# Kernel tuning notes

Hardware: AMD Instinct MI355X
Metric: run time of the kernel (lower is better)

## Reference

```python
import jax, jax.numpy as jnp
import numpy as np

N_NODES = 100000
N_EDGES = 1600000
FEAT_DIM = 64
IN_DIM = FEAT_DIM + 3  # feat + xyz


def setup_inputs() -> dict:
    key = jax.random.key(0)
    k1, k2, k3, k4, k5 = jax.random.split(key, 5)
    xyz = jax.random.normal(k1, (N_NODES, 3), dtype=jnp.float32)
    feat = jax.random.normal(k2, (N_NODES, FEAT_DIM), dtype=jnp.float32)
    edge_index = jax.random.randint(k3, (2, N_EDGES), 0, N_NODES, dtype=jnp.int64)
    # MLP params (Linear stored as [in, out] for x @ W + b)
    W1 = jax.random.normal(k4, (2 * IN_DIM, FEAT_DIM), dtype=jnp.float32) * (1.0 / np.sqrt(2 * IN_DIM))
    b1 = jnp.zeros((FEAT_DIM,), dtype=jnp.float32)
    W2 = jax.random.normal(k5, (FEAT_DIM, FEAT_DIM), dtype=jnp.float32) * (1.0 / np.sqrt(FEAT_DIM))
    b2 = jnp.zeros((FEAT_DIM,), dtype=jnp.float32)
    return {"xyz": xyz, "feat": feat, "edge_index": edge_index,
            "W1": W1, "b1": b1, "W2": W2, "b2": b2}


def reference(xyz, feat, edge_index, W1, b1, W2, b2):
    # node features: cat([feat, xyz]) -> [N, C+3]
    x = jnp.concatenate([feat, xyz], axis=-1)
    src = edge_index[0]  # j (source / neighbor)
    dst = edge_index[1]  # i (target, aggregation index)
    x_i = x[dst]                       # [E, C+3]
    x_j = x[src]                       # [E, C+3]
    # EdgeConv message: mlp(cat([x_i, x_j - x_i]))
    m = jnp.concatenate([x_i, x_j - x_i], axis=-1)   # [E, 2*(C+3)]
    h = jax.nn.relu(m @ W1 + b1) @ W2 + b2           # [E, C]
    n = x.shape[0]
    agg = jax.ops.segment_max(h, dst, num_segments=n)  # [N, C]
    # nodes with no incoming edges get 0 (matches PyG scatter-max fill)
    deg = jax.ops.segment_sum(jnp.ones((dst.shape[0],), h.dtype), dst, num_segments=n)
    return jnp.where(deg[:, None] > 0, agg, jnp.zeros_like(agg))
```

## Files before the change

### kernel.cpp

```cpp
#include <hip/hip_runtime.h>
#include <stdint.h>

#define N_NODES 100000
#define FEAT 64
#define NB 64
#define SC_CHUNK 8192
#define NBKT 1563
#define BKT_CAP 1400
#define RVN 6
#define BIAS 512.0f

typedef __attribute__((ext_vector_type(8))) _Float16 half8;
typedef __attribute__((ext_vector_type(2))) _Float16 half2v;
typedef __attribute__((ext_vector_type(2))) __fp16 fp16x2;
typedef __attribute__((ext_vector_type(4))) float f32x4;

__device__ __forceinline__ uint32_t enc_key(float f) {
    uint32_t u = __float_as_uint(f);
    return (u & 0x80000000u) ? ~u : (u | 0x80000000u);
}
__device__ __forceinline__ float dec_key(uint32_t k) {
    return __uint_as_float((k & 0x80000000u) ? (k & 0x7FFFFFFFu) : ~k);
}
__device__ __forceinline__ uint32_t pk_f16(float a, float b) {
    union { fp16x2 h; uint32_t u; } cv;
    cv.h = __builtin_amdgcn_cvt_pkrtz(a, b);
    return cv.u;
}

#define W2T_OFF 0
#define AMB_OFF 4096
#define BM_OFF  8384
#define W2P_OFF 12672
#define U_OFF   16384
#define V_OFF   (U_OFF + N_NODES * FEAT / 2)
#define GCNT_OFF (U_OFF + N_NODES * FEAT)
#define SRT_OFF  (GCNT_OFF + 2048)

__global__ __launch_bounds__(256) void transform_kernel(
    const float* __restrict__ W1, const float* __restrict__ W2,
    float* __restrict__ ws, int full)
{
    int i = blockIdx.x * 256 + threadIdx.x;
    if (full && i < 2048)
        ((uint32_t*)ws)[GCNT_OFF + i] = 0u;
    if (i < 4096) {
        int c2 = i >> 6, c = i & 63;
        ws[W2T_OFF + i] = W2[c * 64 + c2];
    } else if (full && i < 8384) {
        int j = i - 4096;
        ws[AMB_OFF + j] = W1[j] - W1[j + 67 * 64];
    } else if (full && i < 12672) {
        int j = i - 8384;
        ws[BM_OFF + j] = W1[j + 67 * 64];
    } else if (full && i < 16768) {
        int p = i - 12672;
        int j = p & 7, c2lo = (p >> 3) & 15, quad = (p >> 7) & 3;
        int h = (p >> 9) & 1, n4 = (p >> 10) & 3;
        int k = h * 32 + quad * 8 + j;
        int n = n4 * 16 + c2lo;
        ((_Float16*)(ws + W2P_OFF))[p] = (_Float16)W2[k * 64 + n];
    }
}

__global__ __launch_bounds__(256, 4) void nodebkt_kernel(
    const float* __restrict__ xyz, const float* __restrict__ feat,
    const float* __restrict__ b1, const float* __restrict__ ws,
    uint16_t* __restrict__ U, uint16_t* __restrict__ V, int nN,
    const int* __restrict__ ei, uint32_t* __restrict__ gcnt,
    uint32_t* __restrict__ sorted, int nE, int nBkt)
{
    __shared__ uint32_t hist[NBKT];

    int t = threadIdx.x;

    if ((int)blockIdx.x < nBkt) {
        int e0 = blockIdx.x * SC_CHUNK;
        int cnt = min(SC_CHUNK, nE - e0);
        int cnt4 = cnt & ~3;

        for (int i = t; i < NBKT; i += 256) hist[i] = 0;
        __syncthreads();
        for (int i = t * 4; i < cnt4; i += 1024) {
            uint4 d4 = *(const uint4*)(ei + nE + e0 + i);
            atomicAdd(&hist[d4.x >> 6], 1u);
            atomicAdd(&hist[d4.y >> 6], 1u);
            atomicAdd(&hist[d4.z >> 6], 1u);
            atomicAdd(&hist[d4.w >> 6], 1u);
        }
        for (int i = cnt4 + t; i < cnt; i += 256)
            atomicAdd(&hist[ei[nE + e0 + i] >> 6], 1u);
        __syncthreads();
        for (int b = t; b < NBKT; b += 256) {
            uint32_t c = hist[b];
            hist[b] = c ? atomicAdd(&gcnt[b], c) : 0u;
        }
        __syncthreads();
        for (int i = t * 4; i < cnt4; i += 1024) {
            uint4 s4 = *(const uint4*)(ei + e0 + i);
            uint4 d4 = *(const uint4*)(ei + nE + e0 + i);
            uint32_t sa[4] = {(uint32_t)s4.x, (uint32_t)s4.y, (uint32_t)s4.z, (uint32_t)s4.w};
            uint32_t da[4] = {(uint32_t)d4.x, (uint32_t)d4.y, (uint32_t)d4.z, (uint32_t)d4.w};
            #pragma unroll
            for (int k = 0; k < 4; ++k) {
                uint32_t b = da[k] >> 6;
                uint32_t pos = atomicAdd(&hist[b], 1u);
                if (pos < BKT_CAP)
                    sorted[(size_t)b * BKT_CAP + pos] = sa[k] | ((da[k] & 63u) << 20);
            }
        }
        for (int i = cnt4 + t; i < cnt; i += 256) {
            uint32_t src = (uint32_t)ei[e0 + i];
            uint32_t dst = (uint32_t)ei[nE + e0 + i];
            uint32_t b = dst >> 6;
            uint32_t pos = atomicAdd(&hist[b], 1u);
            if (pos < BKT_CAP)
                sorted[(size_t)b * BKT_CAP + pos] = src | ((dst & 63u) << 20);
        }
        return;
    }

    int nb = blockIdx.x - nBkt;
    int half = nb & 1;
    int n = (nb >> 1) * 256 + t;
    if (n >= nN) return;
    const float* __restrict__ W = ws + (half ? BM_OFF : AMB_OFF);

    float acc[FEAT];
    if (half == 0) {
        #pragma unroll
        for (int c = 0; c < FEAT; ++c) acc[c] = b1[c];
    } else {
        #pragma unroll
        for (int c = 0; c < FEAT; ++c) acc[c] = 0.0f;
    }

    const float* f = feat + (size_t)n * FEAT;
    #pragma unroll 1
    for (int k = 0; k < 64; k += 4) {
        float4 x4 = *(const float4*)(f + k);
        float xv[4] = {x4.x, x4.y, x4.z, x4.w};
        #pragma unroll
        for (int q = 0; q < 4; ++q) {
            const float* __restrict__ w = W + (k + q) * 64;
            #pragma unroll
            for (int c = 0; c < FEAT; ++c)
                acc[c] = fmaf(xv[q], w[c], acc[c]);
        }
    }
    const float* p = xyz + (size_t)n * 3;
    #pragma unroll
    for (int k3 = 0; k3 < 3; ++k3) {
        float xv = p[k3];
        const float* __restrict__ w = W + (64 + k3) * 64;
        #pragma unroll
        for (int c = 0; c < FEAT; ++c)
            acc[c] = fmaf(xv, w[c], acc[c]);
    }
    uint4* outp = (uint4*)((half ? V : U) + (size_t)n * FEAT);
    #pragma unroll
    for (int q = 0; q < 8; ++q) {
        uint4 o;
        o.x = pk_f16(acc[8*q + 0], acc[8*q + 1]);
        o.y = pk_f16(acc[8*q + 2], acc[8*q + 3]);
        o.z = pk_f16(acc[8*q + 4], acc[8*q + 5]);
        o.w = pk_f16(acc[8*q + 6], acc[8*q + 7]);
        outp[q] = o;
    }
}

#define LOADE(G, DSV, VV0, VV1, UU0, UU1) do {                               \
        int e_c_ = min((G) + el, cnt - 1);                                   \
        uint32_t val_ = ssrt[e_c_];                                          \
        DSV = *(const uint4*)(ssrt + (G) + quad * 4);                        \
        int src_ = (int)(val_ & 0xFFFFFu);                                   \
        const uint32_t* vr_ = (const uint32_t*)(V + (size_t)src_ * FEAT);    \
        VV0 = *(const uint4*)(vr_ + quad * 4);                               \
        VV1 = *(const uint4*)(vr_ + 16 + quad * 4);                          \
        const uint32_t* ur_ = ushare + (int)(val_ >> 20) * 32;               \
        UU0 = *(const uint4*)(ur_ + quad * 4);                               \
        UU1 = *(const uint4*)(ur_ + 16 + quad * 4);                          \
    } while (0)

__global__ __launch_bounds__(256) void agg_kernel(
    const uint32_t* __restrict__ gcnt, const uint32_t* __restrict__ sorted,
    const uint16_t* __restrict__ U, const uint16_t* __restrict__ V,
    const float* __restrict__ ws_w2p, const float* __restrict__ b2,
    float* __restrict__ out, int nN)
{
    __shared__ int      lmax[NB * 65];
    __shared__ uint32_t ushare[NB * 32];
    __shared__ uint32_t ssrt[BKT_CAP + 16];
    __shared__ uint32_t shist[NB];

    int bkt = blockIdx.x;
    int nb0 = bkt * NB;
    int rows = min(NB, nN - nb0);
    int cnt = min((int)gcnt[bkt], BKT_CAP);
    int t = threadIdx.x;

    for (int i = t; i < NB * 65; i += 256) lmax[i] = 0;
    if (t < NB) shist[t] = 0;
    {
        const uint4* usrc4 = (const uint4*)(U + (size_t)nb0 * FEAT);
        for (int i = t; i < rows * 8; i += 256) ((uint4*)ushare)[i] = usrc4[i];
    }
    const uint32_t* bsrc = sorted + (size_t)bkt * BKT_CAP;
    __syncthreads();

    uint32_t rv[RVN];
    #pragma unroll
    for (int j = 0; j < RVN; ++j) {
        int i = t + j * 256;
        if (i < cnt) {
            uint32_t v = bsrc[i];
            rv[j] = v;
            atomicAdd(&shist[v >> 20], 1u);
        }
    }
    __syncthreads();
    if (t < NB) {
        uint32_t v = shist[t];
        uint32_t run = v;
        #pragma unroll
        for (int d = 1; d < 64; d <<= 1) {
            uint32_t x = (uint32_t)__shfl_up((int)run, (unsigned)d, 64);
            if (t >= d) run += x;
        }
        shist[t] = run - v;
    }
    __syncthreads();
    #pragma unroll
    for (int j = 0; j < RVN; ++j) {
        int i = t + j * 256;
        if (i < cnt) {
            uint32_t v = rv[j];
            uint32_t pos = atomicAdd(&shist[v >> 20], 1u);
            ssrt[pos] = v;
        }
    }
    __syncthreads();

    int lane = t & 63;
    int wave = t >> 6;
    int el = lane & 15, quad = lane >> 4;

    const uint4* w2p = (const uint4*)ws_w2p;
    union { uint4 u4; half8 h8; } bfr[8];
    #pragma unroll
    for (int q8 = 0; q8 < 8; ++q8)
        bfr[q8].u4 = w2p[(q8 * 4 + quad) * 16 + el];
    float b2v[4];
    #pragma unroll
    for (int n4 = 0; n4 < 4; ++n4) b2v[n4] = b2[n4 * 16 + el] + BIAS;

    const half2v zero2 = {(_Float16)0.0f, (_Float16)0.0f};

    uint4 dsv_c, vv_c0, vv_c1, uu_c0, uu_c1;
    int g = wave * 16;
    if (g < cnt) LOADE(g, dsv_c, vv_c0, vv_c1, uu_c0, uu_c1);

    #pragma unroll 1
    for (; g < cnt; g += 64) {
        int gn = g + 64;
        int gl = (gn < cnt) ? gn : g;
        uint4 dsv_n, vv_n0, vv_n1, uu_n0, uu_n1;
        LOADE(gl, dsv_n, vv_n0, vv_n1, uu_n0, uu_n1);

        union { uint4 u4; half8 h8; } afr[2];
        #pragma unroll
        for (int h = 0; h < 2; ++h) {
            uint4 uu = h ? uu_c1 : uu_c0;
            uint4 vv = h ? vv_c1 : vv_c0;
            uint32_t ua[4] = {uu.x, uu.y, uu.z, uu.w};
            uint32_t va[4] = {vv.x, vv.y, vv.z, vv.w};
            uint32_t pk[4];
            #pragma unroll
            for (int p = 0; p < 4; ++p) {
                union { uint32_t u; half2v h2; } cu, cv2, ct;
                cu.u = ua[p]; cv2.u = va[p];
                ct.h2 = __builtin_elementwise_max(cu.h2 + cv2.h2, zero2);
                pk[p] = ct.u;
            }
            afr[h].u4 = make_uint4(pk[0], pk[1], pk[2], pk[3]);
        }

        f32x4 acc[4];
        #pragma unroll
        for (int n4 = 0; n4 < 4; ++n4)
            acc[n4] = (f32x4){b2v[n4], b2v[n4], b2v[n4], b2v[n4]};
        #pragma unroll
        for (int n4 = 0; n4 < 4; ++n4) {
            acc[n4] = __builtin_amdgcn_mfma_f32_16x16x32_f16(afr[0].h8, bfr[n4*2+0].h8, acc[n4], 0, 0, 0);
            acc[n4] = __builtin_amdgcn_mfma_f32_16x16x32_f16(afr[1].h8, bfr[n4*2+1].h8, acc[n4], 0, 0, 0);
        }

        int d0 = (int)(dsv_c.x >> 20), d1 = (int)(dsv_c.y >> 20);
        int d2 = (int)(dsv_c.z >> 20), d3 = (int)(dsv_c.w >> 20);
        int eb = g + quad * 4;
        bool ok0 = eb < cnt, ok1 = eb + 1 < cnt;
        bool ok2 = eb + 2 < cnt, ok3 = eb + 3 < cnt;
        bool m0 = (d0 == d1) & ok1;
        bool m1 = (d1 == d2) & ok2;
        bool m2 = (d2 == d3) & ok3;
        #pragma unroll
        for (int n4 = 0; n4 < 4; ++n4) {
            if (m0) acc[n4][1] = fmaxf(acc[n4][1], acc[n4][0]);
            if (m1) acc[n4][2] = fmaxf(acc[n4][2], acc[n4][1]);
            if (m2) acc[n4][3] = fmaxf(acc[n4][3], acc[n4][2]);
        }
        if (ok0 & !m0) {
            #pragma unroll
            for (int n4 = 0; n4 < 4; ++n4)
                atomicMax(&lmax[d0 * 65 + n4 * 16 + el], __float_as_int(acc[n4][0]));
        }
        if (ok1 & !m1) {
            #pragma unroll
            for (int n4 = 0; n4 < 4; ++n4)
                atomicMax(&lmax[d1 * 65 + n4 * 16 + el], __float_as_int(acc[n4][1]));
        }
        if (ok2 & !m2) {
            #pragma unroll
            for (int n4 = 0; n4 < 4; ++n4)
                atomicMax(&lmax[d2 * 65 + n4 * 16 + el], __float_as_int(acc[n4][2]));
        }
        if (ok3) {
            #pragma unroll
            for (int n4 = 0; n4 < 4; ++n4)
                atomicMax(&lmax[d3 * 65 + n4 * 16 + el], __float_as_int(acc[n4][3]));
        }

        dsv_c = dsv_n;
        vv_c0 = vv_n0; vv_c1 = vv_n1;
        uu_c0 = uu_n0; uu_c1 = uu_n1;
    }
    __syncthreads();

    for (int i = t * 4; i < rows * FEAT; i += 1024) {
        int r = i >> 6, c = i & 63;
        int lb = r * 65 + c;
        int k0 = lmax[lb + 0], k1 = lmax[lb + 1];
        int k2 = lmax[lb + 2], k3 = lmax[lb + 3];
        float4 o;
        o.x = k0 ? (__int_as_float(k0) - BIAS) : 0.0f;
        o.y = k1 ? (__int_as_float(k1) - BIAS) : 0.0f;
        o.z = k2 ? (__int_as_float(k2) - BIAS) : 0.0f;
        o.w = k3 ? (__int_as_float(k3) - BIAS) : 0.0f;
        *(float4*)(out + (size_t)(nb0 + r) * FEAT + c) = o;
    }
}
#undef LOADE

__device__ __forceinline__ void rank1_update(
    float* __restrict__ h, float xi, float d,
    const float* __restrict__ A, const float* __restrict__ B)
{
    #pragma unroll
    for (int c = 0; c < FEAT; ++c)
        h[c] = fmaf(xi, A[c], fmaf(d, B[c], h[c]));
}

__global__ __launch_bounds__(256) void edge_fused_kernel(
    const float* __restrict__ xyz, const float* __restrict__ feat,
    const int* __restrict__ ei,
    const float* __restrict__ W1, const float* __restrict__ b1,
    const float* __restrict__ ws, const float* __restrict__ b2,
    uint32_t* __restrict__ keys, int nE)
{
    int e = blockIdx.x * 256 + threadIdx.x;
    if (e >= nE) return;
    int src = ei[e];
    int dst = ei[nE + e];
    const float* __restrict__ W2T = ws + W2T_OFF;

    float h[FEAT];
    #pragma unroll
    for (int c = 0; c < FEAT; ++c) h[c] = b1[c];

    const float* fi = feat + (size_t)dst * FEAT;
    const float* fj = feat + (size_t)src * FEAT;
    #pragma unroll 1
    for (int k = 0; k < 64; k += 4) {
        float4 a = *(const float4*)(fi + k);
        float4 b = *(const float4*)(fj + k);
        rank1_update(h, a.x, b.x - a.x, W1 + (k + 0) * 64, W1 + (67 + k + 0) * 64);
        rank1_update(h, a.y, b.y - a.y, W1 + (k + 1) * 64, W1 + (67 + k + 1) * 64);
        rank1_update(h, a.z, b.z - a.z, W1 + (k + 2) * 64, W1 + (67 + k + 2) * 64);
        rank1_update(h, a.w, b.w - a.w, W1 + (k + 3) * 64, W1 + (67 + k + 3) * 64);
    }
    {
        const float* pi = xyz + (size_t)dst * 3;
        const float* pj = xyz + (size_t)src * 3;
        #pragma unroll
        for (int k3 = 0; k3 < 3; ++k3) {
            float xi = pi[k3];
            rank1_update(h, xi, pj[k3] - xi, W1 + (64 + k3) * 64, W1 + (131 + k3) * 64);
        }
    }
    #pragma unroll
    for (int c = 0; c < FEAT; ++c) h[c] = fmaxf(h[c], 0.0f);

    uint32_t* krow = keys + (size_t)dst * FEAT;
    #pragma unroll 1
    for (int c2 = 0; c2 < FEAT; c2 += 4) {
        float o0 = b2[c2 + 0], o1 = b2[c2 + 1];
        float o2 = b2[c2 + 2], o3 = b2[c2 + 3];
        const float* w0 = W2T + (c2 + 0) * 64;
        const float* w1 = W2T + (c2 + 1) * 64;
        const float* w2 = W2T + (c2 + 2) * 64;
        const float* w3 = W2T + (c2 + 3) * 64;
        #pragma unroll
        for (int c = 0; c < FEAT; ++c) {
            float hv = h[c];
            o0 = fmaf(hv, w0[c], o0);
            o1 = fmaf(hv, w1[c], o1);
            o2 = fmaf(hv, w2[c], o2);
            o3 = fmaf(hv, w3[c], o3);
        }
        uint32_t k0 = enc_key(o0), k1 = enc_key(o1);
        uint32_t k2 = enc_key(o2), k3 = enc_key(o3);
        uint4 cur = *(const uint4*)(krow + c2);
        if (k0 > cur.x) atomicMax(&krow[c2 + 0], k0);
        if (k1 > cur.y) atomicMax(&krow[c2 + 1], k1);
        if (k2 > cur.z) atomicMax(&krow[c2 + 2], k2);
        if (k3 > cur.w) atomicMax(&krow[c2 + 3], k3);
    }
}

__global__ __launch_bounds__(256) void decode_kernel(
    uint32_t* __restrict__ keys, int n4)
{
    int i = blockIdx.x * 256 + threadIdx.x;
    if (i >= n4) return;
    uint4 k = ((const uint4*)keys)[i];
    float4 r;
    r.x = k.x ? dec_key(k.x) : 0.0f;
    r.y = k.y ? dec_key(k.y) : 0.0f;
    r.z = k.z ? dec_key(k.z) : 0.0f;
    r.w = k.w ? dec_key(k.w) : 0.0f;
    ((float4*)keys)[i] = r;
}

extern "C" void kernel_launch(void* const* d_in, const int* in_sizes, int n_in,
                              void* d_out, int out_size, void* d_ws, size_t ws_size,
                              hipStream_t stream)
{
    const float* xyz  = (const float*)d_in[0];
    const float* feat = (const float*)d_in[1];
    const int*   ei   = (const int*)d_in[2];
    const float* W1   = (const float*)d_in[3];
    const float* b1   = (const float*)d_in[4];
    const float* W2   = (const float*)d_in[5];
    const float* b2   = (const float*)d_in[6];

    int nE = in_sizes[2] / 2;
    float* ws = (float*)d_ws;

    size_t need_words = (size_t)SRT_OFF + (size_t)NBKT * BKT_CAP;
    int full = (ws_size >= need_words * 4) ? 1 : 0;

    transform_kernel<<<66, 256, 0, stream>>>(W1, W2, ws, full);

    if (full) {
        uint16_t* U = (uint16_t*)(ws + U_OFF);
        uint16_t* V = (uint16_t*)(ws + V_OFF);
        uint32_t* gcnt   = (uint32_t*)(ws + GCNT_OFF);
        uint32_t* sorted = (uint32_t*)(ws + SRT_OFF);

        int nBkt = (nE + SC_CHUNK - 1) / SC_CHUNK;
        int nodeBlocks = ((N_NODES + 255) / 256) * 2;
        nodebkt_kernel<<<nBkt + nodeBlocks, 256, 0, stream>>>(
            xyz, feat, b1, ws, U, V, N_NODES, ei, gcnt, sorted, nE, nBkt);
        agg_kernel<<<NBKT, 256, 0, stream>>>(
            gcnt, sorted, U, V, ws + W2P_OFF, b2, (float*)d_out, N_NODES);
    } else {
        uint32_t* keys = (uint32_t*)d_out;
        hipMemsetAsync(d_out, 0, (size_t)out_size * sizeof(float), stream);
        edge_fused_kernel<<<(nE + 255) / 256, 256, 0, stream>>>(
            xyz, feat, ei, W1, b1, ws, b2, keys, nE);
        decode_kernel<<<(out_size / 4 + 255) / 256, 256, 0, stream>>>(
            keys, out_size / 4);
    }
}
```

Before: 189.5 us.

## Split fused node/bucket kernel into separate launches with LDS occupancy padding

Separates the combined node-projection and edge-bucketing kernel into two kernels launched back to back on the same stream. The node kernel gets a 2D grid and a large dummy shared-memory array, touched only on a never-taken path, that limits blocks per CU, presumably to reduce register or cache pressure from the 64-float accumulator. This removes the branch divergence between block roles and the shared launch bounds, but loses the overlap the fused launch gave between bucketing and node work and adds one launch.

After: 224.6 us. 1.19x slower.

```diff
diff --git a/kernel.cpp b/kernel.cpp
--- a/kernel.cpp
+++ b/kernel.cpp
@@ -9,6 +9,7 @@
 #define BKT_CAP 1400
 #define RVN 6
 #define BIAS 512.0f
+#define NODE_PAD_WORDS 9600
 
 typedef __attribute__((ext_vector_type(8))) _Float16 half8;
 typedef __attribute__((ext_vector_type(2))) _Float16 half2v;
@@ -63,66 +64,22 @@
     }
 }
 
-__global__ __launch_bounds__(256, 4) void nodebkt_kernel(
+__global__ __launch_bounds__(256) void node_kernel(
     const float* __restrict__ xyz, const float* __restrict__ feat,
     const float* __restrict__ b1, const float* __restrict__ ws,
-    uint16_t* __restrict__ U, uint16_t* __restrict__ V, int nN,
-    const int* __restrict__ ei, uint32_t* __restrict__ gcnt,
-    uint32_t* __restrict__ sorted, int nE, int nBkt)
-{
-    __shared__ uint32_t hist[NBKT];
-
+    uint16_t* __restrict__ U, uint16_t* __restrict__ V, int nN)
+{
+    __shared__ uint32_t occ_pad[NODE_PAD_WORDS];
     int t = threadIdx.x;
-
-    if ((int)blockIdx.x < nBkt) {
-        int e0 = blockIdx.x * SC_CHUNK;
-        int cnt = min(SC_CHUNK, nE - e0);
-        int cnt4 = cnt & ~3;
-
-        for (int i = t; i < NBKT; i += 256) hist[i] = 0;
+    if (nN == -1) {
+        occ_pad[t] = (uint32_t)t;
         __syncthreads();
-        for (int i = t * 4; i < cnt4; i += 1024) {
-            uint4 d4 = *(const uint4*)(ei + nE + e0 + i);
-            atomicAdd(&hist[d4.x >> 6], 1u);
-            atomicAdd(&hist[d4.y >> 6], 1u);
-            atomicAdd(&hist[d4.z >> 6], 1u);
-            atomicAdd(&hist[d4.w >> 6], 1u);
-        }
-        for (int i = cnt4 + t; i < cnt; i += 256)
-            atomicAdd(&hist[ei[nE + e0 + i] >> 6], 1u);
-        __syncthreads();
-        for (int b = t; b < NBKT; b += 256) {
-            uint32_t c = hist[b];
-            hist[b] = c ? atomicAdd(&gcnt[b], c) : 0u;
-        }
-        __syncthreads();
-        for (int i = t * 4; i < cnt4; i += 1024) {
-            uint4 s4 = *(const uint4*)(ei + e0 + i);
-            uint4 d4 = *(const uint4*)(ei + nE + e0 + i);
-            uint32_t sa[4] = {(uint32_t)s4.x, (uint32_t)s4.y, (uint32_t)s4.z, (uint32_t)s4.w};
-            uint32_t da[4] = {(uint32_t)d4.x, (uint32_t)d4.y, (uint32_t)d4.z, (uint32_t)d4.w};
-            #pragma unroll
-            for (int k = 0; k < 4; ++k) {
-                uint32_t b = da[k] >> 6;
-                uint32_t pos = atomicAdd(&hist[b], 1u);
-                if (pos < BKT_CAP)
-                    sorted[(size_t)b * BKT_CAP + pos] = sa[k] | ((da[k] & 63u) << 20);
-            }
-        }
-        for (int i = cnt4 + t; i < cnt; i += 256) {
-            uint32_t src = (uint32_t)ei[e0 + i];
-            uint32_t dst = (uint32_t)ei[nE + e0 + i];
-            uint32_t b = dst >> 6;
-            uint32_t pos = atomicAdd(&hist[b], 1u);
-            if (pos < BKT_CAP)
-                sorted[(size_t)b * BKT_CAP + pos] = src | ((dst & 63u) << 20);
-        }
-        return;
-    }
-
-    int nb = blockIdx.x - nBkt;
-    int half = nb & 1;
-    int n = (nb >> 1) * 256 + t;
+        uint32_t x = occ_pad[(uint32_t)(t * 2654435761u) % NODE_PAD_WORDS];
+        if (x == 0xDEADBEEFu) U[0] = 1;
+    }
+
+    int n = blockIdx.x * 256 + t;
+    int half = blockIdx.y;
     if (n >= nN) return;
     const float* __restrict__ W = ws + (half ? BM_OFF : AMB_OFF);
 
@@ -166,6 +123,57 @@
         o.z = pk_f16(acc[8*q + 4], acc[8*q + 5]);
         o.w = pk_f16(acc[8*q + 6], acc[8*q + 7]);
         outp[q] = o;
+    }
+}
+
+__global__ __launch_bounds__(256) void bucket_kernel(
+    const int* __restrict__ ei, uint32_t* __restrict__ gcnt,
+    uint32_t* __restrict__ sorted, int nE)
+{
+    __shared__ uint32_t hist[NBKT];
+
+    int t = threadIdx.x;
+    int e0 = blockIdx.x * SC_CHUNK;
+    int cnt = min(SC_CHUNK, nE - e0);
+    int cnt4 = cnt & ~3;
+
+    for (int i = t; i < NBKT; i += 256) hist[i] = 0;
+    __syncthreads();
+    for (int i = t * 4; i < cnt4; i += 1024) {
+        uint4 d4 = *(const uint4*)(ei + nE + e0 + i);
+        atomicAdd(&hist[d4.x >> 6], 1u);
+        atomicAdd(&hist[d4.y >> 6], 1u);
+        atomicAdd(&hist[d4.z >> 6], 1u);
+        atomicAdd(&hist[d4.w >> 6], 1u);
+    }
+    for (int i = cnt4 + t; i < cnt; i += 256)
+        atomicAdd(&hist[ei[nE + e0 + i] >> 6], 1u);
+    __syncthreads();
+    for (int b = t; b < NBKT; b += 256) {
+        uint32_t c = hist[b];
+        hist[b] = c ? atomicAdd(&gcnt[b], c) : 0u;
+    }
+    __syncthreads();
+    for (int i = t * 4; i < cnt4; i += 1024) {
+        uint4 s4 = *(const uint4*)(ei + e0 + i);
+        uint4 d4 = *(const uint4*)(ei + nE + e0 + i);
+        uint32_t sa[4] = {(uint32_t)s4.x, (uint32_t)s4.y, (uint32_t)s4.z, (uint32_t)s4.w};
+        uint32_t da[4] = {(uint32_t)d4.x, (uint32_t)d4.y, (uint32_t)d4.z, (uint32_t)d4.w};
+        #pragma unroll
+        for (int k = 0; k < 4; ++k) {
+            uint32_t b = da[k] >> 6;
+            uint32_t pos = atomicAdd(&hist[b], 1u);
+            if (pos < BKT_CAP)
+                sorted[(size_t)b * BKT_CAP + pos] = sa[k] | ((da[k] & 63u) << 20);
+        }
+    }
+    for (int i = cnt4 + t; i < cnt; i += 256) {
+        uint32_t src = (uint32_t)ei[e0 + i];
+        uint32_t dst = (uint32_t)ei[nE + e0 + i];
+        uint32_t b = dst >> 6;
+        uint32_t pos = atomicAdd(&hist[b], 1u);
+        if (pos < BKT_CAP)
+            sorted[(size_t)b * BKT_CAP + pos] = src | ((dst & 63u) << 20);
     }
 }
 
@@ -467,10 +475,10 @@
         uint32_t* gcnt   = (uint32_t*)(ws + GCNT_OFF);
         uint32_t* sorted = (uint32_t*)(ws + SRT_OFF);
 
-        int nBkt = (nE + SC_CHUNK - 1) / SC_CHUNK;
-        int nodeBlocks = ((N_NODES + 255) / 256) * 2;
-        nodebkt_kernel<<<nBkt + nodeBlocks, 256, 0, stream>>>(
-            xyz, feat, b1, ws, U, V, N_NODES, ei, gcnt, sorted, nE, nBkt);
+        dim3 ngrid((N_NODES + 255) / 256, 2);
+        node_kernel<<<ngrid, 256, 0, stream>>>(xyz, feat, b1, ws, U, V, N_NODES);
+        bucket_kernel<<<(nE + SC_CHUNK - 1) / SC_CHUNK, 256, 0, stream>>>(
+            ei, gcnt, sorted, nE);
         agg_kernel<<<NBKT, 256, 0, stream>>>(
             gcnt, sorted, U, V, ws + W2P_OFF, b2, (float*)d_out, N_NODES);
     } else {
```
